# Performance work log

Hardware: AMD Instinct MI355X
Metric: run time of the kernel (lower is better)

The kernel has to match this reference:

```python
import jax, jax.numpy as jnp
import numpy as np

# All unordered pairs of 6 ligand sites (octahedral complex)
PAIRS = np.array([(i, j) for i in range(6) for j in range(i + 1, 6)], dtype=np.int32)  # [15, 2]

B, N_LIGS, D = 32768, 6, 64
IN_DIM = D + 2 * D  # core + lig_i + lig_j = 192
H1, H2 = 64, 32


def setup_inputs() -> dict:
    key = jax.random.key(0)
    ks = jax.random.split(key, 8)
    s = 0.05  # small init scale for numerical sanity
    return {
        "core": jax.random.normal(ks[0], (B, D), dtype=jnp.float32),
        "ligs": jax.random.normal(ks[1], (B, N_LIGS, D), dtype=jnp.float32),
        "W1": jax.random.normal(ks[2], (IN_DIM, H1), dtype=jnp.float32) * s,
        "b1": jnp.zeros((H1,), dtype=jnp.float32),
        "W2": jax.random.normal(ks[3], (H1, H2), dtype=jnp.float32) * s,
        "b2": jnp.zeros((H2,), dtype=jnp.float32),
        "W3": jax.random.normal(ks[4], (H2, 1), dtype=jnp.float32) * s,
        "b3": jnp.zeros((1,), dtype=jnp.float32),
    }


def _mlp(x, W1, b1, W2, b2, W3, b3):
    # Dense(softplus) -> Dense(softplus) -> Dense(1, linear); dropout is identity at inference
    h = jax.nn.softplus(x @ W1 + b1)
    h = jax.nn.softplus(h @ W2 + b2)
    return h @ W3 + b3  # [..., 1]


def reference(core, ligs, W1, b1, W2, b2, W3, b3):
    i_idx = jnp.asarray(PAIRS[:, 0])
    j_idx = jnp.asarray(PAIRS[:, 1])
    P = PAIRS.shape[0]
    li = ligs[:, i_idx, :]  # [B, P, D]
    lj = ligs[:, j_idx, :]  # [B, P, D]
    c = jnp.broadcast_to(core[:, None, :], (core.shape[0], P, core.shape[1]))
    x1 = jnp.concatenate([c, li, lj], axis=-1)  # [B, P, 3D]
    x2 = jnp.concatenate([c, lj, li], axis=-1)  # [B, P, 3D]
    res = 0.5 * (_mlp(x1, W1, b1, W2, b2, W3, b3) + _mlp(x2, W1, b1, W2, b2, W3, b3))  # [B, P, 1]
    return jnp.sum(res, axis=1)  # [B, 1]
```

## Files before the change

kernel.cpp:

```cpp
#include <hip/hip_runtime.h>
#include <hip/hip_fp16.h>
#include <stdint.h>


typedef __attribute__((ext_vector_type(8))) _Float16 f16x8;
typedef __attribute__((ext_vector_type(2))) __fp16   fp16v2;
typedef __attribute__((ext_vector_type(4))) float    f32x4;
typedef __attribute__((ext_vector_type(4))) unsigned int u32x4;

constexpr int   BPB       = 32;
constexpr int   NT        = 1024;
constexpr int   T_STRIDE  = 1680;
constexpr int   WT_RS     = 72;
constexpr int   WT_OFF    = BPB * T_STRIDE;
constexpr int   Y_OFF     = WT_OFF + 192 * WT_RS * 2;
constexpr int   LDS_BYTES = Y_OFF + 128;

constexpr int   WS_W1T   = 0;
constexpr int   WS_W2T   = 24576;
constexpr int   WS_B1    = 28672;
constexpr int   WS_B2    = 28928;
constexpr int   WS_W3    = 29056;
constexpr int   WS_BYTES = 29184;

constexpr float L2E = 1.4426950408889634f;
constexpr float LN2 = 0.6931471805599453f;

constexpr unsigned long long I_BITS =
  (0ull<<0)|(0ull<<3)|(0ull<<6)|(0ull<<9)|(0ull<<12)|
  (1ull<<15)|(1ull<<18)|(1ull<<21)|(1ull<<24)|
  (2ull<<27)|(2ull<<30)|(2ull<<33)|
  (3ull<<36)|(3ull<<39)|(4ull<<42);
constexpr unsigned long long J_BITS =
  (1ull<<0)|(2ull<<3)|(3ull<<6)|(4ull<<9)|(5ull<<12)|
  (2ull<<15)|(3ull<<18)|(4ull<<21)|(5ull<<24)|
  (3ull<<27)|(4ull<<30)|(5ull<<33)|
  (4ull<<36)|(5ull<<39)|(5ull<<42);

__device__ __forceinline__ float sp2(float s) {
  float t = __builtin_amdgcn_exp2f(s);
  return __builtin_amdgcn_logf(1.0f + t);
}

__device__ __forceinline__ __half2 h1pair(__half2 u, __half2 a, __half2 b,
                                          __half2 one2) {
  __half2 s = __hadd2(__hadd2(u, a), b);
  __half2 t = h2exp2(s);
  return h2log2(__hadd2(one2, t));
}

__global__ __launch_bounds__(256)
void prep(const float* __restrict__ W1, const float* __restrict__ b1,
          const float* __restrict__ W2, const float* __restrict__ b2,
          const float* __restrict__ W3, char* __restrict__ ws)
{
  const int t = (int)(blockIdx.x * blockDim.x + threadIdx.x);
  uint16_t* w1t = (uint16_t*)(ws + WS_W1T);
  uint16_t* w2t = (uint16_t*)(ws + WS_W2T);
  float*    b1s = (float*)(ws + WS_B1);
  float*    b2s = (float*)(ws + WS_B2);
  float*    w3s = (float*)(ws + WS_W3);
  if (t < 12288) {
    const int d = t >> 6, n = t & 63;
    const int slab = d >> 6;
    w1t[(slab * 64 + n) * 64 + (d & 63)] =
        __half_as_ushort(__float2half(W1[t] * L2E));
  } else if (t < 14336) {
    const int e = t - 12288;
    const int k = e >> 5, m = e & 31;
    w2t[m * 64 + k] = __half_as_ushort(__float2half(W2[e]));
  } else if (t < 14400) {
    b1s[t - 14336] = b1[t - 14336] * L2E;
  } else if (t < 14432) {
    b2s[t - 14400] = b2[t - 14400] * L2E;
  } else if (t < 14464) {
    w3s[t - 14432] = W3[t - 14432] * LN2;
  }
}

__global__ __launch_bounds__(NT, 8)
void tb_fused(const float* __restrict__ core, const float* __restrict__ ligs,
              const float* __restrict__ b3,   const char* __restrict__ ws,
              float* __restrict__ out)
{
  extern __shared__ char smem[];
  const int tid  = (int)threadIdx.x;
  const int lane = tid & 63;
  const int ln   = lane & 15;
  const int qd   = lane >> 4;
  const int wv   = __builtin_amdgcn_readfirstlane(tid >> 6);
  const int b0   = (int)blockIdx.x * BPB;

  const uint16_t* w2t = (const uint16_t*)(ws + WS_W2T);
  const float*    b1s = (const float*)(ws + WS_B1);
  const float*    b2s = (const float*)(ws + WS_B2);
  const float*    w3s = (const float*)(ws + WS_W3);

  float* yred = (float*)(smem + Y_OFF);

  #pragma unroll
  for (int rep = 0; rep < 3; ++rep) {
    const int c   = tid + rep * NT;
    const int row = c >> 4, col = c & 15;
    *(uint2*)(smem + WT_OFF + row * (WT_RS * 2) + col * 8) =
        *(const uint2*)(ws + WS_W1T + row * 128 + col * 8);
  }
  if (tid < BPB) yred[tid] = 0.0f;
  __syncthreads();

  if (wv < 14) {
    const int xr = wv >> 1;
    const int mt = wv & 1;
    const float* src = (xr == 0)
        ? (core + (size_t)(b0 + mt * 16 + ln) * 64)
        : (ligs + ((size_t)(b0 + mt * 16 + ln) * 6 + (size_t)(xr - 1)) * 64);

    union AF { f16x8 v; fp16v2 p[4]; } Afr[2];
    #pragma unroll
    for (int ks = 0; ks < 2; ++ks) {
      const float4 f0 = *(const float4*)(src + ks * 32 + qd * 8);
      const float4 f1 = *(const float4*)(src + ks * 32 + qd * 8 + 4);
      Afr[ks].p[0] = __builtin_amdgcn_cvt_pkrtz(f0.x, f0.y);
      Afr[ks].p[1] = __builtin_amdgcn_cvt_pkrtz(f0.z, f0.w);
      Afr[ks].p[2] = __builtin_amdgcn_cvt_pkrtz(f1.x, f1.y);
      Afr[ks].p[3] = __builtin_amdgcn_cvt_pkrtz(f1.z, f1.w);
    }

    const int sl_lo = (xr == 0) ? 0 : 1;
    const int sl_hi = (xr == 0) ? 0 : 2;
    #pragma unroll 1
    for (int sl = sl_lo; sl <= sl_hi; ++sl) {
      const int trow = (xr == 0) ? 0 : ((sl == 1) ? xr : 6 + xr);
      #pragma unroll
      for (int nt = 0; nt < 4; ++nt) {
        const float bias = (trow == 0) ? b1s[nt * 16 + ln] : 0.0f;
        f32x4 c = {bias, bias, bias, bias};
        #pragma unroll
        for (int ks = 0; ks < 2; ++ks) {
          const f16x8 Bf = *(const f16x8*)(smem + WT_OFF +
              ((sl * 64 + nt * 16 + ln) * WT_RS + ks * 32 + qd * 8) * 2);
          c = __builtin_amdgcn_mfma_f32_16x16x32_f16(Afr[ks].v, Bf, c, 0, 0, 0);
        }
        #pragma unroll
        for (int reg = 0; reg < 4; ++reg) {
          const int b = mt * 16 + qd * 4 + reg;
          *(uint16_t*)(smem + (size_t)b * T_STRIDE + trow * 128 + (nt * 16 + ln) * 2) =
              __half_as_ushort(__float2half(c[reg]));
        }
      }
    }
  }

  f16x8 W2f[2][2];
  #pragma unroll
  for (int nt = 0; nt < 2; ++nt)
    #pragma unroll
    for (int ks = 0; ks < 2; ++ks)
      W2f[nt][ks] = *(const f16x8*)(w2t + (nt * 16 + ln) * 64 + ks * 32 + qd * 8);
  float b2v[2], w3v[2];
  #pragma unroll
  for (int nt = 0; nt < 2; ++nt) {
    b2v[nt] = b2s[nt * 16 + ln];
    w3v[nt] = w3s[nt * 16 + ln];
  }

  __syncthreads();

  const int mtw = wv & 1;
  const int qr  = wv >> 1;
  const __half2 one2 = __float2half2_rn(1.0f);
  const char* Tb  = smem + (size_t)(mtw * 16 + ln) * T_STRIDE;
  const int koff  = qd * 16;

  union U4 { u32x4 u; __half2 h[4]; };
  U4 hu0, hu1;
  hu0.u = *(const u32x4*)(Tb + koff);
  hu1.u = *(const u32x4*)(Tb + 64 + koff);

  float yacc[4] = {0.f, 0.f, 0.f, 0.f};

  #pragma unroll
  for (int t3 = 0; t3 < 4; ++t3) {
    const int q = qr + 8 * t3;
    const float msk = (q < 30) ? 1.0f : 0.0f;
    const int p  = q >> 1;
    const int iv = (int)((I_BITS >> (3 * p)) & 7ull);
    const int jv = (int)((J_BITS >> (3 * p)) & 7ull);
    const int An = (q & 1) ? jv : iv;
    const int Bn = (q & 1) ? iv : jv;
    const char* TA = Tb + (1 + An) * 128;
    const char* TB = Tb + (7 + Bn) * 128;

    U4 da0, db0, da1, db1;
    da0.u = *(const u32x4*)(TA + koff);
    db0.u = *(const u32x4*)(TB + koff);
    da1.u = *(const u32x4*)(TA + 64 + koff);
    db1.u = *(const u32x4*)(TB + 64 + koff);

    union { f16x8 v; __half2 h[4]; } A0, A1;
    #pragma unroll
    for (int w = 0; w < 4; ++w) A0.h[w] = h1pair(hu0.h[w], da0.h[w], db0.h[w], one2);
    #pragma unroll
    for (int w = 0; w < 4; ++w) A1.h[w] = h1pair(hu1.h[w], da1.h[w], db1.h[w], one2);

    f32x4 c0 = {0.f, 0.f, 0.f, 0.f};
    f32x4 c1 = {0.f, 0.f, 0.f, 0.f};
    c0 = __builtin_amdgcn_mfma_f32_16x16x32_f16(A0.v, W2f[0][0], c0, 0, 0, 0);
    c0 = __builtin_amdgcn_mfma_f32_16x16x32_f16(A1.v, W2f[0][1], c0, 0, 0, 0);
    c1 = __builtin_amdgcn_mfma_f32_16x16x32_f16(A0.v, W2f[1][0], c1, 0, 0, 0);
    c1 = __builtin_amdgcn_mfma_f32_16x16x32_f16(A1.v, W2f[1][1], c1, 0, 0, 0);

    #pragma unroll
    for (int reg = 0; reg < 4; ++reg) {
      yacc[reg] += msk * (sp2(c0[reg] + b2v[0]) * w3v[0]
                        + sp2(c1[reg] + b2v[1]) * w3v[1]);
    }
  }

  #pragma unroll
  for (int reg = 0; reg < 4; ++reg) {
    float v = yacc[reg];
    v += __shfl_xor(v, 1);
    v += __shfl_xor(v, 2);
    v += __shfl_xor(v, 4);
    v += __shfl_xor(v, 8);
    yacc[reg] = v;
  }
  if (ln == 0) {
    #pragma unroll
    for (int reg = 0; reg < 4; ++reg)
      atomicAdd(&yred[mtw * 16 + qd * 4 + reg], yacc[reg]);
  }
  __syncthreads();
  if (tid < BPB) out[b0 + tid] = 0.5f * yred[tid] + 15.0f * b3[0];
}

extern "C" void kernel_launch(void* const* d_in, const int* in_sizes, int n_in,
                              void* d_out, int out_size, void* d_ws, size_t ws_size,
                              hipStream_t stream) {
  const float* core = (const float*)d_in[0];
  const float* ligs = (const float*)d_in[1];
  const float* W1   = (const float*)d_in[2];
  const float* b1   = (const float*)d_in[3];
  const float* W2   = (const float*)d_in[4];
  const float* b2   = (const float*)d_in[5];
  const float* W3   = (const float*)d_in[6];
  const float* b3   = (const float*)d_in[7];
  float* out = (float*)d_out;
  char*  ws  = (char*)d_ws;

  const int B = in_sizes[0] / 64;
  const int grid = B / BPB;

  prep<<<dim3(57), dim3(256), 0, stream>>>(W1, b1, W2, b2, W3, ws);

  (void)hipFuncSetAttribute((const void*)tb_fused,
                            hipFuncAttributeMaxDynamicSharedMemorySize, LDS_BYTES);
  tb_fused<<<dim3(grid), dim3(NT), LDS_BYTES, stream>>>(
      core, ligs, b3, ws, out);
}
```

Measured before the change: 127.0 us.

## Fold core projection into ligand tiles and software-pipeline layer-2 LDS loads

```diff
diff --git a/kernel.cpp b/kernel.cpp
--- a/kernel.cpp
+++ b/kernel.cpp
@@ -10,7 +10,7 @@
 
 constexpr int   BPB       = 32;
 constexpr int   NT        = 1024;
-constexpr int   T_STRIDE  = 1680;
+constexpr int   T_STRIDE  = 1552;
 constexpr int   WT_RS     = 72;
 constexpr int   WT_OFF    = BPB * T_STRIDE;
 constexpr int   Y_OFF     = WT_OFF + 192 * WT_RS * 2;
@@ -42,10 +42,8 @@
   return __builtin_amdgcn_logf(1.0f + t);
 }
 
-__device__ __forceinline__ __half2 h1pair(__half2 u, __half2 a, __half2 b,
-                                          __half2 one2) {
-  __half2 s = __hadd2(__hadd2(u, a), b);
-  __half2 t = h2exp2(s);
+__device__ __forceinline__ __half2 h1pair(__half2 a, __half2 b, __half2 one2) {
+  __half2 t = h2exp2(__hadd2(a, b));
   return h2log2(__hadd2(one2, t));
 }
 
@@ -108,45 +106,52 @@
   if (tid < BPB) yred[tid] = 0.0f;
   __syncthreads();
 
-  if (wv < 14) {
-    const int xr = wv >> 1;
+  if (wv < 12) {
+    const int lg = wv >> 1;
     const int mt = wv & 1;
-    const float* src = (xr == 0)
-        ? (core + (size_t)(b0 + mt * 16 + ln) * 64)
-        : (ligs + ((size_t)(b0 + mt * 16 + ln) * 6 + (size_t)(xr - 1)) * 64);
-
-    union AF { f16x8 v; fp16v2 p[4]; } Afr[2];
+    const float* srcC = core + (size_t)(b0 + mt * 16 + ln) * 64;
+    const float* srcL = ligs + ((size_t)(b0 + mt * 16 + ln) * 6 + (size_t)lg) * 64;
+
+    union AF { f16x8 v; fp16v2 p[4]; } Ac[2], Al[2];
     #pragma unroll
     for (int ks = 0; ks < 2; ++ks) {
-      const float4 f0 = *(const float4*)(src + ks * 32 + qd * 8);
-      const float4 f1 = *(const float4*)(src + ks * 32 + qd * 8 + 4);
-      Afr[ks].p[0] = __builtin_amdgcn_cvt_pkrtz(f0.x, f0.y);
-      Afr[ks].p[1] = __builtin_amdgcn_cvt_pkrtz(f0.z, f0.w);
-      Afr[ks].p[2] = __builtin_amdgcn_cvt_pkrtz(f1.x, f1.y);
-      Afr[ks].p[3] = __builtin_amdgcn_cvt_pkrtz(f1.z, f1.w);
+      const float4 c0 = *(const float4*)(srcC + ks * 32 + qd * 8);
+      const float4 c1 = *(const float4*)(srcC + ks * 32 + qd * 8 + 4);
+      Ac[ks].p[0] = __builtin_amdgcn_cvt_pkrtz(c0.x, c0.y);
+      Ac[ks].p[1] = __builtin_amdgcn_cvt_pkrtz(c0.z, c0.w);
+      Ac[ks].p[2] = __builtin_amdgcn_cvt_pkrtz(c1.x, c1.y);
+      Ac[ks].p[3] = __builtin_amdgcn_cvt_pkrtz(c1.z, c1.w);
+      const float4 l0 = *(const float4*)(srcL + ks * 32 + qd * 8);
+      const float4 l1 = *(const float4*)(srcL + ks * 32 + qd * 8 + 4);
+      Al[ks].p[0] = __builtin_amdgcn_cvt_pkrtz(l0.x, l0.y);
+      Al[ks].p[1] = __builtin_amdgcn_cvt_pkrtz(l0.z, l0.w);
+      Al[ks].p[2] = __builtin_amdgcn_cvt_pkrtz(l1.x, l1.y);
+      Al[ks].p[3] = __builtin_amdgcn_cvt_pkrtz(l1.z, l1.w);
     }
 
-    const int sl_lo = (xr == 0) ? 0 : 1;
-    const int sl_hi = (xr == 0) ? 0 : 2;
-    #pragma unroll 1
-    for (int sl = sl_lo; sl <= sl_hi; ++sl) {
-      const int trow = (xr == 0) ? 0 : ((sl == 1) ? xr : 6 + xr);
+    #pragma unroll
+    for (int nt = 0; nt < 4; ++nt) {
+      const float b1v = b1s[nt * 16 + ln];
+      f32x4 cu = {b1v, b1v, b1v, b1v};
+      f32x4 ca = {0.f, 0.f, 0.f, 0.f};
+      f32x4 cb = {0.f, 0.f, 0.f, 0.f};
       #pragma unroll
-      for (int nt = 0; nt < 4; ++nt) {
-        const float bias = (trow == 0) ? b1s[nt * 16 + ln] : 0.0f;
-        f32x4 c = {bias, bias, bias, bias};
-        #pragma unroll
-        for (int ks = 0; ks < 2; ++ks) {
-          const f16x8 Bf = *(const f16x8*)(smem + WT_OFF +
-              ((sl * 64 + nt * 16 + ln) * WT_RS + ks * 32 + qd * 8) * 2);
-          c = __builtin_amdgcn_mfma_f32_16x16x32_f16(Afr[ks].v, Bf, c, 0, 0, 0);
-        }
-        #pragma unroll
-        for (int reg = 0; reg < 4; ++reg) {
-          const int b = mt * 16 + qd * 4 + reg;
-          *(uint16_t*)(smem + (size_t)b * T_STRIDE + trow * 128 + (nt * 16 + ln) * 2) =
-              __half_as_ushort(__float2half(c[reg]));
-        }
+      for (int ks = 0; ks < 2; ++ks) {
+        const int rb = (nt * 16 + ln) * WT_RS + ks * 32 + qd * 8;
+        const f16x8 B0 = *(const f16x8*)(smem + WT_OFF + (rb           ) * 2);
+        const f16x8 B1 = *(const f16x8*)(smem + WT_OFF + (rb + 64*WT_RS) * 2);
+        const f16x8 B2 = *(const f16x8*)(smem + WT_OFF + (rb +128*WT_RS) * 2);
+        cu = __builtin_amdgcn_mfma_f32_16x16x32_f16(Ac[ks].v, B0, cu, 0, 0, 0);
+        ca = __builtin_amdgcn_mfma_f32_16x16x32_f16(Al[ks].v, B1, ca, 0, 0, 0);
+        cb = __builtin_amdgcn_mfma_f32_16x16x32_f16(Al[ks].v, B2, cb, 0, 0, 0);
+      }
+      #pragma unroll
+      for (int reg = 0; reg < 4; ++reg) {
+        const int b = mt * 16 + qd * 4 + reg;
+        const float uh = 0.5f * cu[reg];
+        char* Tbb = smem + (size_t)b * T_STRIDE + (nt * 16 + ln) * 2;
+        *(uint16_t*)(Tbb + lg * 128)       = __half_as_ushort(__float2half(ca[reg] + uh));
+        *(uint16_t*)(Tbb + (6 + lg) * 128) = __half_as_ushort(__float2half(cb[reg] + uh));
       }
     }
   }
@@ -172,50 +177,59 @@
   const char* Tb  = smem + (size_t)(mtw * 16 + ln) * T_STRIDE;
   const int koff  = qd * 16;
 
+  float yacc[4] = {0.f, 0.f, 0.f, 0.f};
+
   union U4 { u32x4 u; __half2 h[4]; };
-  U4 hu0, hu1;
-  hu0.u = *(const u32x4*)(Tb + koff);
-  hu1.u = *(const u32x4*)(Tb + 64 + koff);
-
-  float yacc[4] = {0.f, 0.f, 0.f, 0.f};
-
+
+  int rowA[4], rowB[4];
+  float msk[4];
   #pragma unroll
   for (int t3 = 0; t3 < 4; ++t3) {
     const int q = qr + 8 * t3;
-    const float msk = (q < 30) ? 1.0f : 0.0f;
+    msk[t3] = (q < 30) ? 1.0f : 0.0f;
     const int p  = q >> 1;
     const int iv = (int)((I_BITS >> (3 * p)) & 7ull);
     const int jv = (int)((J_BITS >> (3 * p)) & 7ull);
-    const int An = (q & 1) ? jv : iv;
-    const int Bn = (q & 1) ? iv : jv;
-    const char* TA = Tb + (1 + An) * 128;
-    const char* TB = Tb + (7 + Bn) * 128;
-
-    U4 da0, db0, da1, db1;
-    da0.u = *(const u32x4*)(TA + koff);
-    db0.u = *(const u32x4*)(TB + koff);
-    da1.u = *(const u32x4*)(TA + 64 + koff);
-    db1.u = *(const u32x4*)(TB + 64 + koff);
-
+    rowA[t3] = ((q & 1) ? jv : iv) * 128;
+    rowB[t3] = (6 + ((q & 1) ? iv : jv)) * 128;
+  }
+
+  auto loadu = [&](int t3, U4& a0, U4& a1, U4& bb0, U4& bb1) {
+    a0.u  = *(const u32x4*)(Tb + rowA[t3] + koff);
+    a1.u  = *(const u32x4*)(Tb + rowA[t3] + 64 + koff);
+    bb0.u = *(const u32x4*)(Tb + rowB[t3] + koff);
+    bb1.u = *(const u32x4*)(Tb + rowB[t3] + 64 + koff);
+  };
+
+  auto compute = [&](const U4& a0, const U4& a1, const U4& bb0, const U4& bb1,
+                     float m) {
     union { f16x8 v; __half2 h[4]; } A0, A1;
     #pragma unroll
-    for (int w = 0; w < 4; ++w) A0.h[w] = h1pair(hu0.h[w], da0.h[w], db0.h[w], one2);
-    #pragma unroll
-    for (int w = 0; w < 4; ++w) A1.h[w] = h1pair(hu1.h[w], da1.h[w], db1.h[w], one2);
-
-    f32x4 c0 = {0.f, 0.f, 0.f, 0.f};
-    f32x4 c1 = {0.f, 0.f, 0.f, 0.f};
+    for (int w = 0; w < 4; ++w) A0.h[w] = h1pair(a0.h[w], bb0.h[w], one2);
+    #pragma unroll
+    for (int w = 0; w < 4; ++w) A1.h[w] = h1pair(a1.h[w], bb1.h[w], one2);
+    f32x4 c0 = {b2v[0], b2v[0], b2v[0], b2v[0]};
+    f32x4 c1 = {b2v[1], b2v[1], b2v[1], b2v[1]};
     c0 = __builtin_amdgcn_mfma_f32_16x16x32_f16(A0.v, W2f[0][0], c0, 0, 0, 0);
     c0 = __builtin_amdgcn_mfma_f32_16x16x32_f16(A1.v, W2f[0][1], c0, 0, 0, 0);
     c1 = __builtin_amdgcn_mfma_f32_16x16x32_f16(A0.v, W2f[1][0], c1, 0, 0, 0);
     c1 = __builtin_amdgcn_mfma_f32_16x16x32_f16(A1.v, W2f[1][1], c1, 0, 0, 0);
-
-    #pragma unroll
-    for (int reg = 0; reg < 4; ++reg) {
-      yacc[reg] += msk * (sp2(c0[reg] + b2v[0]) * w3v[0]
-                        + sp2(c1[reg] + b2v[1]) * w3v[1]);
-    }
-  }
+    const float w3m0 = w3v[0] * m;
+    const float w3m1 = w3v[1] * m;
+    #pragma unroll
+    for (int reg = 0; reg < 4; ++reg)
+      yacc[reg] += sp2(c0[reg]) * w3m0 + sp2(c1[reg]) * w3m1;
+  };
+
+  U4 pa0, pa1, pb0, pb1, na0, na1, nb0, nb1;
+  loadu(0, pa0, pa1, pb0, pb1);
+  loadu(1, na0, na1, nb0, nb1);
+  compute(pa0, pa1, pb0, pb1, msk[0]);
+  loadu(2, pa0, pa1, pb0, pb1);
+  compute(na0, na1, nb0, nb1, msk[1]);
+  loadu(3, na0, na1, nb0, nb1);
+  compute(pa0, pa1, pb0, pb1, msk[2]);
+  compute(na0, na1, nb0, nb1, msk[3]);
 
   #pragma unroll
   for (int reg = 0; reg < 4; ++reg) {
```

Measured after the change: 147.9 us. 1.16x slower.
